# Optimization experiments

Hardware: AMD Instinct MI355X
Metric: run time of the kernel (lower is better)

The kernel has to match this reference:

```python
import jax, jax.numpy as jnp
import numpy as np
import math

B, S, D, H = 2, 2048, 1024, 16
DH = D // H          # 64 head dim
BLK = 64             # SpargeAttn block size
TOPK = 0.5           # fraction of KV blocks kept per query block
NEG = -1e9


def setup_inputs() -> dict:
    key = jax.random.key(0)
    ks = jax.random.split(key, 8)
    s = 0.02
    return {
        "inputs": jax.random.normal(ks[0], (B, S, D), dtype=jnp.float32),
        "ln_g": jnp.ones((D,), jnp.float32),
        "ln_b": jnp.zeros((D,), jnp.float32),
        "Wq": jax.random.normal(ks[1], (D, D), jnp.float32) * s,
        "bq": jnp.zeros((D,), jnp.float32),
        "Wk": jax.random.normal(ks[2], (D, D), jnp.float32) * s,
        "bk": jnp.zeros((D,), jnp.float32),
        "Wv": jax.random.normal(ks[3], (D, D), jnp.float32) * s,
        "bv": jnp.zeros((D,), jnp.float32),
        "Wo": jax.random.normal(ks[4], (D, D), jnp.float32) * s,
        "bo": jnp.zeros((D,), jnp.float32),
    }


def _sparse_topk_attn(q, k, v):
    # q,k,v: [B,H,S,DH]. Block-mean-similarity top-k sparse causal attention
    # (SpargeAttn spas_sage2_attn_meansim_topk, fp32 reference semantics).
    nb = S // BLK
    qm = q.reshape(B, H, nb, BLK, DH).mean(3)          # [B,H,nb,DH]
    km = k.reshape(B, H, nb, BLK, DH).mean(3)
    sim = jnp.einsum('bhqd,bhkd->bhqk', qm, km)        # block similarity
    cblk = jnp.tril(jnp.ones((nb, nb), bool))          # causal block mask
    sim = jnp.where(cblk, sim, NEG)
    kk = max(1, int(math.ceil(TOPK * nb)))
    _, idx = jax.lax.top_k(sim, kk)                    # [B,H,nb,kk]
    blk = jax.nn.one_hot(idx, nb, dtype=jnp.float32).sum(-2) > 0  # [B,H,nb,nb]
    blk = (blk & cblk) | jnp.eye(nb, dtype=bool)       # keep diagonal block
    tok_mask = jnp.repeat(jnp.repeat(blk, BLK, axis=2), BLK, axis=3)  # [B,H,S,S]
    tok_mask = tok_mask & jnp.tril(jnp.ones((S, S), bool))
    scores = jnp.einsum('bhid,bhjd->bhij', q, k) / jnp.float32(math.sqrt(DH))
    scores = jnp.where(tok_mask, scores, NEG)
    p = jax.nn.softmax(scores, axis=-1)
    return jnp.einsum('bhij,bhjd->bhid', p, v)


def reference(inputs, ln_g, ln_b, Wq, bq, Wk, bk, Wv, bv, Wo, bo):
    # pre-norm LayerNorm
    mu = inputs.mean(-1, keepdims=True)
    var = inputs.var(-1, keepdims=True)
    x = (inputs - mu) * jax.lax.rsqrt(var + 1e-5) * ln_g + ln_b
    # QKV projections -> [B,H,S,DH]
    q = (x @ Wq + bq).reshape(B, S, H, DH).transpose(0, 2, 1, 3)
    k = (x @ Wk + bk).reshape(B, S, H, DH).transpose(0, 2, 1, 3)
    v = (x @ Wv + bv).reshape(B, S, H, DH).transpose(0, 2, 1, 3)
    ctx = _sparse_topk_attn(q, k, v)
    ctx = ctx.transpose(0, 2, 1, 3).reshape(B, S, D)
    return ctx @ Wo + bo
```

## Files before the change

kernel.cpp:

```cpp
#include <hip/hip_runtime.h>
#include <stdint.h>

#define DEV static __device__ __forceinline__

typedef __attribute__((ext_vector_type(8))) short s16x8;
typedef __attribute__((ext_vector_type(4))) float f32x4;

constexpr int Bdim = 2, Sdim = 2048, Ddim = 1024, Hdim = 16, DH = 64;
constexpr int Mrows = Bdim * Sdim;
constexpr int NB = 32;
constexpr int SEL_STRIDE = 18;

constexpr size_t OFF_XB    = 0;
constexpr size_t OFF_WTQKV = OFF_XB    + (size_t)Mrows*Ddim*2;
constexpr size_t OFF_WOT   = OFF_WTQKV + (size_t)3072*1024*2;
constexpr size_t OFF_QKV   = OFF_WOT   + (size_t)1024*1024*2;
constexpr size_t OFF_CTX   = OFF_QKV   + (size_t)Mrows*3072*2;
constexpr size_t OFF_XM    = OFF_CTX   + (size_t)Mrows*Ddim*2;
constexpr size_t OFF_QM    = OFF_XM    + (size_t)64*1024*4;
constexpr size_t OFF_KM    = OFF_QM    + (size_t)64*1024*4;
constexpr size_t OFF_BIASQ = OFF_KM    + (size_t)64*1024*4;
constexpr size_t OFF_SEL   = OFF_BIASQ + (size_t)3072*4;
constexpr size_t OFF_PART  = OFF_SEL   + (size_t)1024*SEL_STRIDE*4;

DEV float bf2f(unsigned short u){ union{unsigned int i; float f;} x; x.i = ((unsigned int)u)<<16; return x.f; }
DEV unsigned short f2bf(float f){ union{float f; unsigned int i;} x; x.f=f;
  unsigned int r = x.i + 0x7fffu + ((x.i>>16)&1u); return (unsigned short)(r>>16); }

DEV void gload16(const unsigned short* g, unsigned short* l){
  __builtin_amdgcn_global_load_lds(
      (__attribute__((address_space(1))) void*)(void*)g,
      (__attribute__((address_space(3))) void*)l, 16, 0, 0);
}

DEV unsigned int cvtpk(float a, float b){
  unsigned int r;
  asm("v_cvt_pk_bf16_f32 %0, %1, %2" : "=v"(r) : "v"(a), "v"(b));
  return r;
}

__global__ __launch_bounds__(256) void ln_kernel(const float* __restrict__ inp,
                                                 const float* __restrict__ gam,
                                                 const float* __restrict__ bet,
                                                 unsigned short* __restrict__ xb){
  const int row = blockIdx.x, t = threadIdx.x;
  __shared__ float red[8];
  const float4 v = ((const float4*)(inp + (size_t)row*Ddim))[t];
  float s  = v.x + v.y + v.z + v.w;
  float s2 = v.x*v.x + v.y*v.y + v.z*v.z + v.w*v.w;
#pragma unroll
  for (int mk=32; mk>=1; mk>>=1){ s += __shfl_xor(s, mk); s2 += __shfl_xor(s2, mk); }
  if ((t&63)==0){ red[t>>6] = s; red[4+(t>>6)] = s2; }
  __syncthreads();
  s  = red[0]+red[1]+red[2]+red[3];
  s2 = red[4]+red[5]+red[6]+red[7];
  const float mu  = s * (1.f/Ddim);
  const float var = s2 * (1.f/Ddim) - mu*mu;
  const float rs  = rsqrtf(var + 1e-5f);
  const float4 gv = ((const float4*)gam)[t];
  const float4 bv = ((const float4*)bet)[t];
  float o0 = (v.x-mu)*rs*gv.x + bv.x;
  float o1 = (v.y-mu)*rs*gv.y + bv.y;
  float o2 = (v.z-mu)*rs*gv.z + bv.z;
  float o3 = (v.w-mu)*rs*gv.w + bv.w;
  uint2 u;
  u.x = (unsigned int)f2bf(o0) | ((unsigned int)f2bf(o1)<<16);
  u.y = (unsigned int)f2bf(o2) | ((unsigned int)f2bf(o3)<<16);
  ((uint2*)(xb + (size_t)row*Ddim))[t] = u;
}

__global__ __launch_bounds__(256) void xm_kernel(const float* __restrict__ inp,
                                                 const float* __restrict__ gam,
                                                 const float* __restrict__ bet,
                                                 float* __restrict__ xm){
  const int blk = blockIdx.x, t = threadIdx.x;
  const int w = t>>6, lane = t&63;
  __shared__ float part[4][1024];
  float4 gv[4], bv[4];
#pragma unroll
  for (int p=0;p<4;++p){ gv[p] = ((const float4*)gam)[lane + 64*p];
                         bv[p] = ((const float4*)bet)[lane + 64*p]; }
  float ax[4][4];
#pragma unroll
  for (int p=0;p<4;++p)
#pragma unroll
    for (int c=0;c<4;++c) ax[p][c]=0.f;
  for (int rr=0; rr<16; ++rr){
    const int row = blk*64 + w*16 + rr;
    const float4* rp = (const float4*)(inp + (size_t)row*Ddim);
    float4 v[4]; float s=0.f, s2=0.f;
#pragma unroll
    for (int p=0;p<4;++p){
      v[p] = rp[lane + 64*p];
      s  += v[p].x+v[p].y+v[p].z+v[p].w;
      s2 += v[p].x*v[p].x+v[p].y*v[p].y+v[p].z*v[p].z+v[p].w*v[p].w;
    }
#pragma unroll
    for (int mk=32; mk>=1; mk>>=1){ s += __shfl_xor(s,mk); s2 += __shfl_xor(s2,mk); }
    const float mu = s*(1.f/Ddim);
    const float var = s2*(1.f/Ddim) - mu*mu;
    const float rs = rsqrtf(var + 1e-5f);
#pragma unroll
    for (int p=0;p<4;++p){
      ax[p][0] += (v[p].x-mu)*rs*gv[p].x + bv[p].x;
      ax[p][1] += (v[p].y-mu)*rs*gv[p].y + bv[p].y;
      ax[p][2] += (v[p].z-mu)*rs*gv[p].z + bv[p].z;
      ax[p][3] += (v[p].w-mu)*rs*gv[p].w + bv[p].w;
    }
  }
#pragma unroll
  for (int p=0;p<4;++p){
    float4 o; o.x=ax[p][0]; o.y=ax[p][1]; o.z=ax[p][2]; o.w=ax[p][3];
    ((float4*)&part[w][0])[lane + 64*p] = o;
  }
  __syncthreads();
  float4 r0 = ((float4*)&part[0][0])[t];
  float4 r1 = ((float4*)&part[1][0])[t];
  float4 r2 = ((float4*)&part[2][0])[t];
  float4 r3 = ((float4*)&part[3][0])[t];
  float4 o;
  o.x = (r0.x+r1.x+r2.x+r3.x)*(1.f/64);
  o.y = (r0.y+r1.y+r2.y+r3.y)*(1.f/64);
  o.z = (r0.z+r1.z+r2.z+r3.z)*(1.f/64);
  o.w = (r0.w+r1.w+r2.w+r3.w)*(1.f/64);
  ((float4*)(xm + (size_t)blk*Ddim))[t] = o;
}

__global__ __launch_bounds__(256) void wtrans4_kernel(const float* __restrict__ Wq,
                                                      const float* __restrict__ Wk,
                                                      const float* __restrict__ Wv,
                                                      const float* __restrict__ Wo,
                                                      const float* __restrict__ bq,
                                                      const float* __restrict__ bk,
                                                      const float* __restrict__ bv,
                                                      unsigned short* __restrict__ wtqkv,
                                                      unsigned short* __restrict__ wot,
                                                      float* __restrict__ bqkv){
  __shared__ float tile[32][33];
  const int z = blockIdx.z;
  const float* W = (z==0)?Wq:(z==1)?Wk:(z==2)?Wv:Wo;
  unsigned short* Wt = (z<3) ? (wtqkv + (size_t)z*1024*1024) : wot;
  const int n0 = blockIdx.x*32, k0 = blockIdx.y*32;
  const int t = threadIdx.x, r = t>>5, c = t&31;
  if (z<3 && blockIdx.x==0 && blockIdx.y==0){
    const float* bb = (z==0)?bq:(z==1)?bk:bv;
#pragma unroll
    for (int i=0;i<4;++i) bqkv[z*1024 + t + 256*i] = bb[t + 256*i];
  }
#pragma unroll
  for (int i=0;i<4;++i) tile[r+8*i][c] = W[(size_t)(k0 + r + 8*i)*1024 + n0 + c];
  __syncthreads();
#pragma unroll
  for (int i=0;i<4;++i) Wt[(size_t)(n0 + r + 8*i)*1024 + k0 + c] = f2bf(tile[c][r+8*i]);
}

__global__ __launch_bounds__(256) void qmkm_part(const float* __restrict__ xm,
    const float* __restrict__ Wq, const float* __restrict__ Wk,
    float* __restrict__ part){
  const int c  = blockIdx.x*256 + threadIdx.x;
  const int rg = blockIdx.y >> 3, ks = blockIdx.y & 7;
  const int z  = blockIdx.z;
  const float* W = z ? Wk : Wq;
  const int r0 = rg*16, k0 = ks*128;
  float acc[16];
#pragma unroll
  for (int r=0;r<16;++r) acc[r]=0.f;
  for (int k=0;k<128;k+=4){
    const float wv0 = W[(size_t)(k0+k  )*1024 + c];
    const float wv1 = W[(size_t)(k0+k+1)*1024 + c];
    const float wv2 = W[(size_t)(k0+k+2)*1024 + c];
    const float wv3 = W[(size_t)(k0+k+3)*1024 + c];
#pragma unroll
    for (int r=0;r<16;++r){
      const float4 xv = *(const float4*)&xm[(size_t)(r0+r)*1024 + k0 + k];
      acc[r] = fmaf(xv.w, wv3, fmaf(xv.z, wv2, fmaf(xv.y, wv1, fmaf(xv.x, wv0, acc[r]))));
    }
  }
  float* dst = part + (((size_t)z*8 + ks)*64 + r0)*1024 + c;
#pragma unroll
  for (int r=0;r<16;++r) dst[(size_t)r*1024] = acc[r];
}

__global__ __launch_bounds__(256) void qmkm_reduce(const float* __restrict__ part,
    const float* __restrict__ bq, const float* __restrict__ bk,
    float* __restrict__ qm, float* __restrict__ km){
  const int idx = blockIdx.x*256 + threadIdx.x;
  const int z = blockIdx.y;
  const int c = idx & 1023, r = idx >> 10;
  const float* p = part + ((size_t)z*8*64*1024) + (size_t)r*1024 + c;
  float s = 0.f;
#pragma unroll
  for (int ks=0; ks<8; ++ks) s += p[(size_t)ks*64*1024];
  s += z ? bk[c] : bq[c];
  (z ? km : qm)[(size_t)r*1024 + c] = s;
}

__global__ __launch_bounds__(256) void topk_kernel(const float* __restrict__ qm,
                                                   const float* __restrict__ km,
                                                   int* __restrict__ sel){
  const int bhq = blockIdx.x;
  const int qb = bhq & 31, h = (bhq>>5) & 15, b = bhq >> 9;
  const int t = threadIdx.x;
  __shared__ float sim[32];
  __shared__ int keep[32];
  const int kb = t>>3, l8 = t&7;
  float acc = 0.f;
  if (kb <= qb){
    const float* qv = qm + (size_t)(b*32 + qb)*1024 + h*64;
    const float* kv = km + (size_t)(b*32 + kb)*1024 + h*64;
#pragma unroll
    for (int d=0; d<8; ++d) acc += qv[l8*8+d] * kv[l8*8+d];
  }
  acc += __shfl_xor(acc,1); acc += __shfl_xor(acc,2); acc += __shfl_xor(acc,4);
  if (l8==0) sim[kb] = (kb<=qb) ? acc : -1e30f;
  __syncthreads();
  if (t < 32){
    int k2 = t; int ok = 0;
    if (k2 <= qb){
      float sv = sim[k2]; int rank = 0;
      for (int j=0;j<=qb;++j){
        float sj = sim[j];
        rank += (sj > sv) || (sj == sv && j < k2);
      }
      ok = (rank < 16) || (k2 == qb);
    }
    keep[t] = ok;
  }
  __syncthreads();
  if (t == 0){
    int* dstp = sel + (size_t)bhq * SEL_STRIDE;
    int c = 0;
    for (int j=0;j<32;++j) if (keep[j]) dstp[1+c++] = j;
    dstp[0] = c;
  }
}

#define G_STAGE(bsel, kofs) do { \
  gload16(A0 + (kofs), ldsA + (bsel)*4096 + (wid*2+0)*512); \
  gload16(A1 + (kofs), ldsA + (bsel)*4096 + (wid*2+1)*512); \
  gload16(B0 + (kofs), ldsB + (bsel)*4096 + (wid*2+0)*512); \
  gload16(B1 + (kofs), ldsB + (bsel)*4096 + (wid*2+1)*512); \
} while(0)

#define G_COMPUTE(bsel) do { \
  s16x8 af[4], bfr[4]; \
  _Pragma("unroll") \
  for (int mi=0;mi<4;++mi){ \
    int row = wr*64 + mi*16 + rl; \
    af[mi] = *(const s16x8*)((char*)ldsA + (bsel)*8192 + row*64 + ((g ^ ((row>>1)&3))<<4)); \
  } \
  _Pragma("unroll") \
  for (int ni=0;ni<4;++ni){ \
    int row = wc*64 + ni*16 + rl; \
    bfr[ni] = *(const s16x8*)((char*)ldsB + (bsel)*8192 + row*64 + ((g ^ ((row>>1)&3))<<4)); \
  } \
  _Pragma("unroll") \
  for (int mi=0;mi<4;++mi) \
    _Pragma("unroll") \
    for (int ni=0;ni<4;++ni) \
      acc[mi][ni] = __builtin_amdgcn_mfma_f32_16x16x32_bf16(af[mi], bfr[ni], acc[mi][ni], 0,0,0); \
} while(0)

template<int OUT_BF16>
__global__ __launch_bounds__(256) void gemm_bt(const unsigned short* __restrict__ A,
                                               const unsigned short* __restrict__ Bt,
                                               const float* __restrict__ bias,
                                               void* __restrict__ C, int N){
  constexpr int K = 1024;
  constexpr int NT = K/32;
  __shared__ unsigned short ldsA[2*128*32];
  __shared__ unsigned short ldsB[2*128*32];
  const int t = threadIdx.x, lane = t & 63, wid = t >> 6;
  const int wr = wid >> 1, wc = wid & 1;
  const int rl = lane & 15, g = lane >> 4;

  const int nbx = gridDim.x, nby = gridDim.y;
  const int id  = blockIdx.y * nbx + blockIdx.x;
  const int xcd = id & 7, j = id >> 3;
  const int MBP = nby >> 2, NBP = nbx >> 1;
  const int mg = xcd >> 1, ng = xcd & 1;
  const int m0 = (mg*MBP + (j % MBP)) * 128;
  const int n0 = (ng*NBP + (j / MBP)) * 128;

  const f32x4 ZERO4 = {0.f,0.f,0.f,0.f};
  f32x4 acc[4][4];
#pragma unroll
  for (int i=0;i<4;++i)
#pragma unroll
    for (int j2=0;j2<4;++j2) acc[i][j2] = ZERO4;

  const int slot0 = wid*128 + lane, slot1 = slot0 + 64;
  const int sr0 = slot0>>2, sc0 = slot0&3;
  const int sr1 = slot1>>2, sc1 = slot1&3;
  const unsigned short* A0 = A  + (size_t)(m0 + sr0)*K + (sc0 ^ ((sr0>>1)&3))*8;
  const unsigned short* A1 = A  + (size_t)(m0 + sr1)*K + (sc1 ^ ((sr1>>1)&3))*8;
  const unsigned short* B0 = Bt + (size_t)(n0 + sr0)*K + (sc0 ^ ((sr0>>1)&3))*8;
  const unsigned short* B1 = Bt + (size_t)(n0 + sr1)*K + (sc1 ^ ((sr1>>1)&3))*8;

  G_STAGE(0, 0);

  for (int ti=0; ti<NT; ++ti){
    const int cur = ti & 1;
    if (ti+1 < NT){
      G_STAGE(cur^1, (ti+1)*32);
      asm volatile("s_waitcnt vmcnt(4)" ::: "memory");
    } else {
      asm volatile("s_waitcnt vmcnt(0)" ::: "memory");
    }
    __builtin_amdgcn_s_barrier();
    __builtin_amdgcn_sched_barrier(0);
    G_COMPUTE(cur);
    __builtin_amdgcn_sched_barrier(0);
    __builtin_amdgcn_s_barrier();
  }

  const int r4 = g*4;
#pragma unroll
  for (int mi=0;mi<4;++mi){
#pragma unroll
    for (int ni=0;ni<4;++ni){
      int col = n0 + wc*64 + ni*16 + rl;
      float bb = bias[col];
#pragma unroll
      for (int e=0;e<4;++e){
        int row = m0 + wr*64 + mi*16 + r4 + e;
        float v = acc[mi][ni][e] + bb;
        if (OUT_BF16) ((unsigned short*)C)[(size_t)row*N + col] = f2bf(v);
        else          ((float*)C)[(size_t)row*N + col] = v;
      }
    }
  }
}

__global__ __launch_bounds__(256) void attn_kernel(const unsigned short* __restrict__ qkv,
                                                   const int* __restrict__ sel,
                                                   unsigned short* __restrict__ ctx){
  const int id = blockIdx.x;
  const int xcd = id & 7, jj = id >> 3;
  const int bh = xcd + 8*(jj/24);
  const int tau = jj % 24;
  const int h = bh & 15, b = bh >> 4;
  int qbl[2]; int nq;
  if (tau < 8){ qbl[0]=tau; qbl[1]=15-tau; nq=2; }
  else        { qbl[0]=tau+8; qbl[1]=0;    nq=1; }

  const int t = threadIdx.x, wid = t >> 6, lane = t & 63;
  const int rl = lane & 15, g = lane >> 4;
  const int q_local = wid*16 + rl;

  __shared__ unsigned short K_s[2][4096];
  __shared__ unsigned short V_s[2][4096];

  const int jst = t >> 2, cq = t & 3;
  const int r2 = t >> 3, dq = t & 7;
  const unsigned short* kbase = qkv + (size_t)(b*Sdim + jst)*3072 + 1024 + h*DH + cq*16;
  const unsigned short* vbase = qkv + (size_t)(b*Sdim + 2*r2)*3072 + 2048 + h*DH + dq*8;
  const int kwb0 = jst*128 + (((cq*2  ) ^ (jst&7))<<4);
  const int kwb1 = jst*128 + (((cq*2+1) ^ (jst&7))<<4);
  const f32x4 ZERO4 = {0.f,0.f,0.f,0.f};

  const int src0 = (rl + 16*((2*g  ) & 3)) << 2;
  const int src1 = (rl + 16*((2*g+1) & 3)) << 2;
  const bool hsel = (g >> 1);

  for (int iq=0; iq<nq; ++iq){
    const int qb = qbl[iq];
    const int* selrow = sel + (size_t)(((b*Hdim)+h)*NB + qb) * SEL_STRIDE;
    const int ns = selrow[0];

    const int qg0 = b*Sdim + qb*64 + q_local;
    const unsigned short* qbase = qkv + (size_t)qg0*3072 + h*DH;
    s16x8 qa[2];
#pragma unroll
    for (int kk=0; kk<2; ++kk){
      s16x8 raw = *(const s16x8*)(qbase + kk*32 + g*8);
      s16x8 qq;
#pragma unroll
      for (int e=0;e<8;++e) qq[e] = (short)f2bf(bf2f((unsigned short)raw[e]) * 0.125f);
      qa[kk] = qq;
    }

    f32x4 o[4];
    float m_r = -3.0e38f, l_r = 0.f;
#pragma unroll
    for (int f=0; f<4; ++f) o[f] = ZERO4;

    __syncthreads();

    int kb = selrow[1];
    s16x8 kr0, kr1, vr0, vr1;
    {
      const size_t off = (size_t)kb*64*3072;
      kr0 = *(const s16x8*)(kbase + off);
      kr1 = *(const s16x8*)(kbase + off + 8);
      vr0 = *(const s16x8*)(vbase + off);
      vr1 = *(const s16x8*)(vbase + off + 3072);
    }

    for (int it=0; it<ns; ++it){
      const int buf = it & 1;
      unsigned short* Kw = &K_s[buf][0];
      unsigned short* Vw = &V_s[buf][0];
      *(s16x8*)((char*)Kw + kwb0) = kr0;
      *(s16x8*)((char*)Kw + kwb1) = kr1;
#pragma unroll
      for (int e=0;e<8;++e){
        const int d1 = dq*8 + e;
        const int sw = (d1&7) ^ (d1>>3);
        const unsigned int pr = (unsigned int)(unsigned short)vr0[e]
                              | ((unsigned int)(unsigned short)vr1[e] << 16);
        *(unsigned int*)((char*)Vw + d1*128 + ((4*r2) ^ (sw<<4))) = pr;
      }
      const int kbcur = kb;
      if (it+1 < ns){
        kb = selrow[2+it];
        const size_t off = (size_t)kb*64*3072;
        kr0 = *(const s16x8*)(kbase + off);
        kr1 = *(const s16x8*)(kbase + off + 8);
        vr0 = *(const s16x8*)(vbase + off);
        vr1 = *(const s16x8*)(vbase + off + 3072);
      }
      __syncthreads();

      f32x4 sfT[4];
#pragma unroll
      for (int f=0;f<4;++f) sfT[f] = ZERO4;
      __builtin_amdgcn_s_setprio(1);
#pragma unroll
      for (int kk=0;kk<2;++kk){
#pragma unroll
        for (int f=0;f<4;++f){
          const int jr = f*16 + rl;
          s16x8 kf = *(const s16x8*)((char*)Kw + jr*128 + (((kk*4+g) ^ (jr&7))<<4));
          sfT[f] = __builtin_amdgcn_mfma_f32_16x16x32_bf16(kf, qa[kk], sfT[f], 0,0,0);
        }
      }
      __builtin_amdgcn_s_setprio(0);
      if (kbcur == qb){
#pragma unroll
        for (int f=0;f<4;++f)
#pragma unroll
          for (int e=0;e<4;++e){
            const int j2 = f*16 + g*4 + e;
            if (j2 > q_local) sfT[f][e] = -1e9f;
          }
      }
      {
        float mx = sfT[0][0];
#pragma unroll
        for (int f=0;f<4;++f)
#pragma unroll
          for (int e=0;e<4;++e) mx = fmaxf(mx, sfT[f][e]);
        mx = fmaxf(mx, __shfl_xor(mx, 16));
        mx = fmaxf(mx, __shfl_xor(mx, 32));
        const float mn = fmaxf(m_r, mx);
        const float al = __expf(m_r - mn);
        m_r = mn;
        float rs = 0.f;
#pragma unroll
        for (int f=0;f<4;++f)
#pragma unroll
          for (int e=0;e<4;++e){
            const float p = __expf(sfT[f][e] - mn);
            sfT[f][e] = p; rs += p;
          }
        rs += __shfl_xor(rs, 16);
        rs += __shfl_xor(rs, 32);
        l_r = l_r*al + rs;
#pragma unroll
        for (int f=0;f<4;++f)
#pragma unroll
          for (int e=0;e<4;++e) o[f][e] *= al;
      }

      unsigned int plo[4], phi[4];
#pragma unroll
      for (int f=0;f<4;++f){
        plo[f] = cvtpk(sfT[f][0], sfT[f][1]);
        phi[f] = cvtpk(sfT[f][2], sfT[f][3]);
      }

#pragma unroll
      for (int kk=0;kk<2;++kk){
        const int f0 = 2*kk, f1 = 2*kk+1;
        unsigned int a0, b0, w0, w1, w2, w3;
        a0 = __builtin_amdgcn_ds_bpermute(src0, plo[f0]);
        b0 = __builtin_amdgcn_ds_bpermute(src0, plo[f1]);
        w0 = hsel ? b0 : a0;
        a0 = __builtin_amdgcn_ds_bpermute(src0, phi[f0]);
        b0 = __builtin_amdgcn_ds_bpermute(src0, phi[f1]);
        w1 = hsel ? b0 : a0;
        a0 = __builtin_amdgcn_ds_bpermute(src1, plo[f0]);
        b0 = __builtin_amdgcn_ds_bpermute(src1, plo[f1]);
        w2 = hsel ? b0 : a0;
        a0 = __builtin_amdgcn_ds_bpermute(src1, phi[f0]);
        b0 = __builtin_amdgcn_ds_bpermute(src1, phi[f1]);
        w3 = hsel ? b0 : a0;
        union { unsigned int u[4]; s16x8 v; } pfc;
        pfc.u[0] = w0; pfc.u[1] = w1; pfc.u[2] = w2; pfc.u[3] = w3;
        const s16x8 pf = pfc.v;
        __builtin_amdgcn_s_setprio(1);
#pragma unroll
        for (int f=0;f<4;++f){
          const int d = f*16 + rl;
          const int sw = (d&7) ^ (d>>3);
          s16x8 vf = *(const s16x8*)((char*)Vw + d*128 + ((64*kk + 16*g) ^ (sw<<4)));
          o[f] = __builtin_amdgcn_mfma_f32_16x16x32_bf16(vf, pf, o[f], 0,0,0);
        }
        __builtin_amdgcn_s_setprio(0);
      }
    }

    {
      const float inv = 1.f / l_r;
      unsigned short* crow = ctx + (size_t)qg0*Ddim + h*DH;
#pragma unroll
      for (int f=0;f<4;++f){
        uint2 st;
        st.x = (unsigned int)f2bf(o[f][0]*inv) | ((unsigned int)f2bf(o[f][1]*inv)<<16);
        st.y = (unsigned int)f2bf(o[f][2]*inv) | ((unsigned int)f2bf(o[f][3]*inv)<<16);
        *(uint2*)(crow + f*16 + g*4) = st;
      }
    }
  }
}

extern "C" void kernel_launch(void* const* d_in, const int* in_sizes, int n_in,
                              void* d_out, int out_size, void* d_ws, size_t ws_size,
                              hipStream_t stream){
  (void)in_sizes; (void)n_in; (void)out_size; (void)ws_size;
  const float* inp  = (const float*)d_in[0];
  const float* ln_g = (const float*)d_in[1];
  const float* ln_b = (const float*)d_in[2];
  const float* Wq   = (const float*)d_in[3];
  const float* bq   = (const float*)d_in[4];
  const float* Wk   = (const float*)d_in[5];
  const float* bk   = (const float*)d_in[6];
  const float* Wv   = (const float*)d_in[7];
  const float* bv   = (const float*)d_in[8];
  const float* Wo   = (const float*)d_in[9];
  const float* bo   = (const float*)d_in[10];

  char* ws = (char*)d_ws;
  unsigned short* xb    = (unsigned short*)(ws + OFF_XB);
  unsigned short* wtqkv = (unsigned short*)(ws + OFF_WTQKV);
  unsigned short* wot   = (unsigned short*)(ws + OFF_WOT);
  unsigned short* qkvb  = (unsigned short*)(ws + OFF_QKV);
  unsigned short* ctx   = (unsigned short*)(ws + OFF_CTX);
  float* xm   = (float*)(ws + OFF_XM);
  float* qm   = (float*)(ws + OFF_QM);
  float* km   = (float*)(ws + OFF_KM);
  float* bqkv = (float*)(ws + OFF_BIASQ);
  int*   sel  = (int*)(ws + OFF_SEL);
  float* part = (float*)(ws + OFF_PART);

  ln_kernel<<<Mrows, 256, 0, stream>>>(inp, ln_g, ln_b, xb);
  xm_kernel<<<64, 256, 0, stream>>>(inp, ln_g, ln_b, xm);
  wtrans4_kernel<<<dim3(32,32,4), 256, 0, stream>>>(Wq, Wk, Wv, Wo, bq, bk, bv, wtqkv, wot, bqkv);
  qmkm_part<<<dim3(4,32,2), 256, 0, stream>>>(xm, Wq, Wk, part);
  qmkm_reduce<<<dim3(256,2), 256, 0, stream>>>(part, bq, bk, qm, km);
  topk_kernel<<<1024, 256, 0, stream>>>(qm, km, sel);
  gemm_bt<1><<<dim3(24,32), 256, 0, stream>>>(xb, wtqkv, bqkv, (void*)qkvb, 3072);
  attn_kernel<<<768, 256, 0, stream>>>(qkvb, sel, ctx);
  gemm_bt<0><<<dim3(8,32), 256, 0, stream>>>(ctx, wot, bo, d_out, 1024);
}
```

Before: 146.7 us.

## Fold softmax scale into QKV GEMM epilogue and use lazy exp2 rescaling

The QKV GEMM epilogue now multiplies Q by 1/sqrt(64)*log2(e), so the attention kernel loads Q directly without per-element rescaling and computes exponentials with raw v_exp_f32. The online softmax only rescales the running max and accumulators when some lane's new max exceeds the old one by more than 8, and the row-sum shuffle reduction moves from every iteration to a single reduction at the end. This cuts transcendental and shuffle work in the attention inner loop. In exchange, Q is rounded to bf16 after scaling, and deferred rescaling lets unnormalized values grow by up to 2^8, which changes numerics slightly.

```diff
diff --git a/kernel.cpp b/kernel.cpp
--- a/kernel.cpp
+++ b/kernel.cpp
@@ -10,6 +10,8 @@
 constexpr int Mrows = Bdim * Sdim;
 constexpr int NB = 32;
 constexpr int SEL_STRIDE = 18;
+
+#define QSCALE 0.18033688011112042f
 
 constexpr size_t OFF_XB    = 0;
 constexpr size_t OFF_WTQKV = OFF_XB    + (size_t)Mrows*Ddim*2;
@@ -36,6 +38,12 @@
 DEV unsigned int cvtpk(float a, float b){
   unsigned int r;
   asm("v_cvt_pk_bf16_f32 %0, %1, %2" : "=v"(r) : "v"(a), "v"(b));
+  return r;
+}
+
+DEV float exp2fast(float x){
+  float r;
+  asm("v_exp_f32 %0, %1" : "=v"(r) : "v"(x));
   return r;
 }
 
@@ -261,7 +269,7 @@
       acc[mi][ni] = __builtin_amdgcn_mfma_f32_16x16x32_bf16(af[mi], bfr[ni], acc[mi][ni], 0,0,0); \
 } while(0)
 
-template<int OUT_BF16>
+template<int OUT_BF16, int SCALEQ>
 __global__ __launch_bounds__(256) void gemm_bt(const unsigned short* __restrict__ A,
                                                const unsigned short* __restrict__ Bt,
                                                const float* __restrict__ bias,
@@ -321,10 +329,11 @@
     for (int ni=0;ni<4;++ni){
       int col = n0 + wc*64 + ni*16 + rl;
       float bb = bias[col];
+      float sc = (SCALEQ && col < 1024) ? QSCALE : 1.0f;
 #pragma unroll
       for (int e=0;e<4;++e){
         int row = m0 + wr*64 + mi*16 + r4 + e;
-        float v = acc[mi][ni][e] + bb;
+        float v = (acc[mi][ni][e] + bb) * sc;
         if (OUT_BF16) ((unsigned short*)C)[(size_t)row*N + col] = f2bf(v);
         else          ((float*)C)[(size_t)row*N + col] = v;
       }
@@ -371,17 +380,11 @@
     const int qg0 = b*Sdim + qb*64 + q_local;
     const unsigned short* qbase = qkv + (size_t)qg0*3072 + h*DH;
     s16x8 qa[2];
-#pragma unroll
-    for (int kk=0; kk<2; ++kk){
-      s16x8 raw = *(const s16x8*)(qbase + kk*32 + g*8);
-      s16x8 qq;
-#pragma unroll
-      for (int e=0;e<8;++e) qq[e] = (short)f2bf(bf2f((unsigned short)raw[e]) * 0.125f);
-      qa[kk] = qq;
-    }
+    qa[0] = *(const s16x8*)(qbase + g*8);
+    qa[1] = *(const s16x8*)(qbase + 32 + g*8);
 
     f32x4 o[4];
-    float m_r = -3.0e38f, l_r = 0.f;
+    float m_r = -3.0e38f, l_p = 0.f;
 #pragma unroll
     for (int f=0; f<4; ++f) o[f] = ZERO4;
 
@@ -453,24 +456,34 @@
           for (int e=0;e<4;++e) mx = fmaxf(mx, sfT[f][e]);
         mx = fmaxf(mx, __shfl_xor(mx, 16));
         mx = fmaxf(mx, __shfl_xor(mx, 32));
-        const float mn = fmaxf(m_r, mx);
-        const float al = __expf(m_r - mn);
-        m_r = mn;
-        float rs = 0.f;
-#pragma unroll
-        for (int f=0;f<4;++f)
-#pragma unroll
-          for (int e=0;e<4;++e){
-            const float p = __expf(sfT[f][e] - mn);
-            sfT[f][e] = p; rs += p;
-          }
-        rs += __shfl_xor(rs, 16);
-        rs += __shfl_xor(rs, 32);
-        l_r = l_r*al + rs;
-#pragma unroll
-        for (int f=0;f<4;++f)
-#pragma unroll
-          for (int e=0;e<4;++e) o[f][e] *= al;
+        if (__any(mx > m_r + 8.0f)){
+          const float mn = fmaxf(m_r, mx);
+          const float al = exp2fast(m_r - mn);
+          m_r = mn;
+          float rs = 0.f;
+#pragma unroll
+          for (int f=0;f<4;++f)
+#pragma unroll
+            for (int e=0;e<4;++e){
+              const float p = exp2fast(sfT[f][e] - mn);
+              sfT[f][e] = p; rs += p;
+            }
+          l_p = l_p*al + rs;
+#pragma unroll
+          for (int f=0;f<4;++f)
+#pragma unroll
+            for (int e=0;e<4;++e) o[f][e] *= al;
+        } else {
+          float rs = 0.f;
+#pragma unroll
+          for (int f=0;f<4;++f)
+#pragma unroll
+            for (int e=0;e<4;++e){
+              const float p = exp2fast(sfT[f][e] - m_r);
+              sfT[f][e] = p; rs += p;
+            }
+          l_p += rs;
+        }
       }
 
       unsigned int plo[4], phi[4];
@@ -512,6 +525,9 @@
     }
 
     {
+      float l_r = l_p;
+      l_r += __shfl_xor(l_r, 16);
+      l_r += __shfl_xor(l_r, 32);
       const float inv = 1.f / l_r;
       unsigned short* crow = ctx + (size_t)qg0*Ddim + h*DH;
 #pragma unroll
@@ -560,7 +576,7 @@
   qmkm_part<<<dim3(4,32,2), 256, 0, stream>>>(xm, Wq, Wk, part);
   qmkm_reduce<<<dim3(256,2), 256, 0, stream>>>(part, bq, bk, qm, km);
   topk_kernel<<<1024, 256, 0, stream>>>(qm, km, sel);
-  gemm_bt<1><<<dim3(24,32), 256, 0, stream>>>(xb, wtqkv, bqkv, (void*)qkvb, 3072);
+  gemm_bt<1,1><<<dim3(24,32), 256, 0, stream>>>(xb, wtqkv, bqkv, (void*)qkvb, 3072);
   attn_kernel<<<768, 256, 0, stream>>>(qkvb, sel, ctx);
-  gemm_bt<0><<<dim3(8,32), 256, 0, stream>>>(ctx, wot, bo, d_out, 1024);
-}
+  gemm_bt<0,0><<<dim3(8,32), 256, 0, stream>>>(ctx, wot, bo, d_out, 1024);
+}
```

New measurement: 160.4 us. +9.3%, slower.
